# Kernel optimization log

Measured on AMD Instinct MI355X. Metric: run time of the kernel, lower is better.

Reference implementation:

```python
import jax, jax.numpy as jnp
import numpy as np

LAM = 0.95  # config.discount_lambda


def setup_inputs() -> dict:
    key = jax.random.key(0)
    k1, k2, k3 = jax.random.split(key, 3)
    T, B = 16, 524288  # imag_horizon + 1, flattened batch*length
    reward = jax.random.normal(k1, (T, B), jnp.float32) * 0.1
    value = jax.random.normal(k2, (T, B), jnp.float32)
    # cont-head mean in [0, 1) scaled by find_discount ~ 0.997
    discount = 0.997 * jax.random.uniform(k3, (T, B), jnp.float32)
    return {"reward": reward, "value": value, "discount": discount}


def reference(reward, value, discount):
    """Faithful jax version of ImagBehavior.lambda_return.

    torch loop (i = T-2 .. 0):
        curr = acc_last * lam + value[i+1] * (1 - lam)
        curr = reward[i] + discount[i] * curr
    then flip to time order. Here expressed as a single reverse lax.scan.
    Returns target of shape [T-1, B] in time order (indices 0 .. T-2).
    """
    def step(acc, xs):
        r, d, v_next = xs
        acc = r + d * (LAM * acc + (1.0 - LAM) * v_next)
        return acc, acc

    bootstrap = value[-1]  # [B]
    xs = (reward[:-1], discount[:-1], value[1:])  # each [T-1, B]
    _, target = jax.lax.scan(step, bootstrap, xs, reverse=True)
    return target  # [T-1, B]
```

## Files before the change

### kernel.cpp

```cpp
#include <hip/hip_runtime.h>


constexpr int   T_STEPS = 16;
constexpr float LAM     = 0.95f;

__global__ __launch_bounds__(256, 4)
void ImagBehavior_67284957659345_kernel(const float2* __restrict__ reward,
                                        const float2* __restrict__ value,
                                        const float2* __restrict__ discount,
                                        float2* __restrict__ out,
                                        int Bv ) {
    int idx = blockIdx.x * blockDim.x + threadIdx.x;
    if (idx >= Bv) return;

    float2 r[T_STEPS - 1];
    float2 d[T_STEPS - 1];
    float2 v[T_STEPS];

    v[T_STEPS - 1] = value[(T_STEPS - 1) * Bv + idx];
#pragma unroll
    for (int t = T_STEPS - 2; t >= 0; --t) {
        r[t] = reward[t * Bv + idx];
        d[t] = discount[t * Bv + idx];
        if (t >= 1) v[t] = value[t * Bv + idx];
    }

    float2 acc = v[T_STEPS - 1];
#pragma unroll
    for (int t = T_STEPS - 2; t >= 0; --t) {
        const float2 vn = v[t + 1];
        acc.x = r[t].x + d[t].x * (LAM * acc.x + (1.0f - LAM) * vn.x);
        acc.y = r[t].y + d[t].y * (LAM * acc.y + (1.0f - LAM) * vn.y);
        out[t * Bv + idx] = acc;
    }
}

extern "C" void kernel_launch(void* const* d_in, const int* in_sizes, int n_in,
                              void* d_out, int out_size, void* d_ws, size_t ws_size,
                              hipStream_t stream) {
    const float2* reward   = (const float2*)d_in[0];
    const float2* value    = (const float2*)d_in[1];
    const float2* discount = (const float2*)d_in[2];
    float2*       out      = (float2*)d_out;

    const int B  = in_sizes[0] / T_STEPS;
    const int Bv = B / 2;

    const int block = 256;
    const int grid  = (Bv + block - 1) / block;

    ImagBehavior_67284957659345_kernel<<<grid, block, 0, stream>>>(
        reward, value, discount, out, Bv);
}
```

Measured before the change: 127.3 us.

## Stream timesteps through a 4-deep register ring buffer and raise occupancy

Instead of loading all 16 timesteps of reward, discount and value into registers up front, each thread keeps a 4-slot rolling buffer. It prefetches timestep t-4 while computing timestep t. This lowers register pressure so launch bounds can request 8 blocks per SM instead of 4, trading deep per-thread prefetch for more resident waves to hide memory latency. The kernel is memory-bound, so the gain depends on whether more occupancy beats the lost per-thread memory-level parallelism.

```diff
diff --git a/kernel.cpp b/kernel.cpp
--- a/kernel.cpp
+++ b/kernel.cpp
@@ -3,8 +3,9 @@
 
 constexpr int   T_STEPS = 16;
 constexpr float LAM     = 0.95f;
+constexpr int   W       = 4;
 
-__global__ __launch_bounds__(256, 4)
+__global__ __launch_bounds__(256, 8)
 void ImagBehavior_67284957659345_kernel(const float2* __restrict__ reward,
                                         const float2* __restrict__ value,
                                         const float2* __restrict__ discount,
@@ -13,25 +14,40 @@
     int idx = blockIdx.x * blockDim.x + threadIdx.x;
     if (idx >= Bv) return;
 
-    float2 r[T_STEPS - 1];
-    float2 d[T_STEPS - 1];
-    float2 v[T_STEPS];
+    float2 r[W], d[W], v[W];
 
-    v[T_STEPS - 1] = value[(T_STEPS - 1) * Bv + idx];
+    float2 acc = value[(T_STEPS - 1) * Bv + idx];
+
+#pragma unroll
+    for (int j = 0; j < W; ++j) {
+        const int t = T_STEPS - 2 - j;
+        r[t & (W - 1)] = reward[t * Bv + idx];
+        d[t & (W - 1)] = discount[t * Bv + idx];
+        v[t & (W - 1)] = value[t * Bv + idx];
+    }
+
+    float2 v_next = acc;
+
 #pragma unroll
     for (int t = T_STEPS - 2; t >= 0; --t) {
-        r[t] = reward[t * Bv + idx];
-        d[t] = discount[t * Bv + idx];
-        if (t >= 1) v[t] = value[t * Bv + idx];
-    }
+        const int s = t & (W - 1);
+        const float2 rt    = r[s];
+        const float2 dt    = d[s];
+        const float2 vt1   = v_next;
+        const float2 vtcur = v[s];
 
-    float2 acc = v[T_STEPS - 1];
-#pragma unroll
-    for (int t = T_STEPS - 2; t >= 0; --t) {
-        const float2 vn = v[t + 1];
-        acc.x = r[t].x + d[t].x * (LAM * acc.x + (1.0f - LAM) * vn.x);
-        acc.y = r[t].y + d[t].y * (LAM * acc.y + (1.0f - LAM) * vn.y);
+        const int tp = t - W;
+        if (tp >= 0) {
+            r[tp & (W - 1)] = reward[tp * Bv + idx];
+            d[tp & (W - 1)] = discount[tp * Bv + idx];
+            if (tp >= 1) v[tp & (W - 1)] = value[tp * Bv + idx];
+        }
+
+        acc.x = rt.x + dt.x * (LAM * acc.x + (1.0f - LAM) * vt1.x);
+        acc.y = rt.y + dt.y * (LAM * acc.y + (1.0f - LAM) * vt1.y);
         out[t * Bv + idx] = acc;
+
+        v_next = vtcur;
     }
 }
 
```

Result: no change. 126.8 us (-0.4%).
